# Kernel optimization log

Measured on AMD Instinct MI355X. Metric: run time of the kernel, lower is better.

Reference implementation:

```python
import jax, jax.numpy as jnp
import numpy as np

PAD_IDX = 0


def setup_inputs() -> dict:
    key = jax.random.key(0)
    ks = jax.random.split(key, 6)
    nentries, entry_size, bsize, nemb, vocab = 8000, 32, 64, 256, 50000
    keys = jax.random.randint(ks[0], (nentries,), 0, vocab)
    entries = jax.random.randint(ks[1], (nentries, entry_size), 0, vocab)
    query = jax.random.normal(ks[2], (bsize, nemb), dtype=jnp.float32)
    wordemb = jax.random.normal(ks[3], (vocab, nemb), dtype=jnp.float32)
    qproj_w = jax.random.uniform(ks[4], (nemb, nemb), jnp.float32, -0.1, 0.1)
    qproj_b = jnp.zeros((nemb,), jnp.float32)
    return dict(keys=keys, entries=entries, query=query, wordemb=wordemb,
                qproj_w=qproj_w, qproj_b=qproj_b)


def _embed(ids, wordemb):
    # F.embedding with padding_idx: gathered rows at pad_idx are zeroed
    return wordemb[ids] * (ids != PAD_IDX)[..., None].astype(wordemb.dtype)


def reference(keys, entries, query, wordemb, qproj_w, qproj_b):
    keys_e = _embed(keys, wordemb)       # (m, d)
    ents_e = _embed(entries, wordemb)    # (m, n, d)
    # --- single hop (max_hops = 1) ---
    # value_atten: query attends over the n tokens inside each entry
    vq = query @ qproj_w.T + qproj_b                       # (b, d)
    logits_v = jnp.einsum('ik,mnk->imn', vq, ents_e)       # (b, m, n)
    prob_v = jax.nn.softmax(logits_v, axis=-1)
    ents = jnp.einsum('imn,mnk->imk', prob_v, ents_e)      # (b, m, d)
    # entry_atten: query attends over entries via their keys
    logits_e = jnp.einsum('ik,jk->ij', query, keys_e)      # (b, m)
    prob_e = jax.nn.softmax(logits_e, axis=-1)
    o_k = prob_e @ keys_e                                  # (b, d)
    combined = jnp.einsum('bm,bme->be', prob_e, ents)      # (b, d)
    # return (us[-1], prob_list[-1], combined_entries)
    return o_k, logits_e, combined
```

## Files before the change

### kernel.cpp

```cpp
#include <hip/hip_runtime.h>
#include <math.h>

#define B 64
#define D 256
#define M 8000
#define N 32
#define LG_LD 8000
#define EPB 16
#define NBLK (M / EPB)
#define VOCAB 50000

typedef unsigned short u16;
typedef __bf16 bf16x8 __attribute__((ext_vector_type(8)));
typedef float fx4 __attribute__((ext_vector_type(4)));

#define STR_E  264
#define STR_P  40

static __device__ __forceinline__ u16 f2bf(float x) {
    unsigned int u = __float_as_uint(x);
    u += 0x7FFFu + ((u >> 16) & 1u);
    return (u16)(u >> 16);
}
static __device__ __forceinline__ float bf2f(u16 h) {
    return __uint_as_float(((unsigned)h) << 16);
}
static __device__ __forceinline__ uint4 pack8(float4 va, float4 vb, float msk) {
    unsigned p0 = (unsigned)f2bf(va.x * msk) | ((unsigned)f2bf(va.y * msk) << 16);
    unsigned p1 = (unsigned)f2bf(va.z * msk) | ((unsigned)f2bf(va.w * msk) << 16);
    unsigned p2 = (unsigned)f2bf(vb.x * msk) | ((unsigned)f2bf(vb.y * msk) << 16);
    unsigned p3 = (unsigned)f2bf(vb.z * msk) | ((unsigned)f2bf(vb.w * msk) << 16);
    return make_uint4(p0, p1, p2, p3);
}

__global__ __launch_bounds__(256) void k_prep_all(const int* __restrict__ keys,
                                                  const float* __restrict__ emb,
                                                  const float* __restrict__ q,
                                                  const float* __restrict__ W,
                                                  const float* __restrict__ bias,
                                                  u16* __restrict__ embb,
                                                  u16* __restrict__ qbf,
                                                  u16* __restrict__ keb,
                                                  u16* __restrict__ vqb) {
    __shared__ float qs[D];
    int t = threadIdx.x, bid = blockIdx.x;
    if (bid < 6250) {
        size_t idx = (size_t)bid * 2048 + (size_t)t * 8;
        float4 v0 = *(const float4*)(emb + idx);
        float4 v1 = *(const float4*)(emb + idx + 4);
        float msk = (idx < D) ? 0.f : 1.f;
        uint4 pk = pack8(v0, v1, msk);
        *(uint4*)(embb + idx) = pk;
    } else if (bid < 7250) {
        int c = (bid - 6250) * 256 + t;
        int j = c >> 5, sp = c & 31;
        int id = keys[j];
        const float* rp = emb + (size_t)id * D + sp * 8;
        float4 v0 = *(const float4*)rp;
        float4 v1 = *(const float4*)(rp + 4);
        float msk = (id != 0) ? 1.f : 0.f;
        uint4 pk = pack8(v0, v1, msk);
        *(uint4*)(keb + (size_t)j * D + sp * 8) = pk;
    } else if (bid < 7258) {
        size_t idx = (size_t)(bid - 7250) * 2048 + (size_t)t * 8;
        float4 v0 = *(const float4*)(q + idx);
        float4 v1 = *(const float4*)(q + idx + 4);
        uint4 pk = pack8(v0, v1, 1.f);
        *(uint4*)(qbf + idx) = pk;
    } else {
        int b = bid - 7258;
        qs[t] = q[b * D + t];
        __syncthreads();
        const float* wr = W + t * D;
        float acc = bias[t];
#pragma unroll 8
        for (int k = 0; k < D; k += 4) {
            float4 w4 = *(const float4*)(wr + k);
            acc += qs[k] * w4.x + qs[k + 1] * w4.y + qs[k + 2] * w4.z + qs[k + 3] * w4.w;
        }
        vqb[b * D + t] = f2bf(acc);
    }
}

__global__ __launch_bounds__(256, 2) void k_heavy_f(const int* __restrict__ entries,
                                                    const u16* __restrict__ embb,
                                                    const u16* __restrict__ vqb,
                                                    const u16* __restrict__ qbf,
                                                    const u16* __restrict__ keb,
                                                    float* __restrict__ lg,
                                                    u16* __restrict__ numCp,
                                                    u16* __restrict__ numKp,
                                                    float* __restrict__ mLp,
                                                    float* __restrict__ denLp) {
    __shared__ __align__(16) u16 sEu[2][N * STR_E];
    __shared__ __align__(16) u16 sETu[2][64 * 136];
    __shared__ __align__(16) u16 sPu[B * STR_P];
    __shared__ float sw[EPB][B];

    int t = threadIdx.x;
    int lane = t & 63, l = lane & 15, q = lane >> 4, w = t >> 6;
    int b0 = 16 * w;
    int sp = t & 31, n0 = t >> 5;
    int m0 = blockIdx.x * EPB;
    int bb = t & 63, y = t >> 6;

    int idc[4], idn[4];
    uint4 pfF[4];
#pragma unroll
    for (int i = 0; i < 4; ++i) idc[i] = entries[m0 * N + n0 + 8 * i];
#pragma unroll
    for (int i = 0; i < 4; ++i)
        pfF[i] = *(const uint4*)(embb + (size_t)idc[i] * D + sp * 8);

    fx4 zero4 = {0.f, 0.f, 0.f, 0.f};
    fx4 aL = zero4;
#pragma unroll
    for (int s = 0; s < 8; ++s) {
        bf16x8 a  = *(const bf16x8*)(qbf + (size_t)(b0 + l) * D + 32 * s + 8 * q);
        bf16x8 bq = *(const bf16x8*)(keb + (size_t)(m0 + l) * D + 32 * s + 8 * q);
        aL = __builtin_amdgcn_mfma_f32_16x16x32_bf16(a, bq, aL, 0, 0, 0);
    }
#pragma unroll
    for (int r = 0; r < 4; ++r)
        lg[(size_t)(b0 + 4 * q + r) * LG_LD + m0 + l] = aL[r];

#pragma unroll
    for (int r = 0; r < 4; ++r) {
        float m_ = aL[r];
        m_ = fmaxf(m_, __shfl_xor(m_, 1));
        m_ = fmaxf(m_, __shfl_xor(m_, 2));
        m_ = fmaxf(m_, __shfl_xor(m_, 4));
        m_ = fmaxf(m_, __shfl_xor(m_, 8));
        float wv = __expf(aL[r] - m_);
        sw[l][b0 + 4 * q + r] = wv;
        float d_ = wv;
        d_ += __shfl_xor(d_, 1);
        d_ += __shfl_xor(d_, 2);
        d_ += __shfl_xor(d_, 4);
        d_ += __shfl_xor(d_, 8);
        if (l == 0) {
            mLp[blockIdx.x * B + b0 + 4 * q + r] = m_;
            denLp[blockIdx.x * B + b0 + 4 * q + r] = d_;
        }
    }

    bf16x8 vqf[8];
#pragma unroll
    for (int s = 0; s < 8; ++s)
        vqf[s] = *(const bf16x8*)(vqb + (b0 + l) * D + 32 * s + 8 * q);

    fx4 acc[16];
#pragma unroll
    for (int dt = 0; dt < 16; ++dt) acc[dt] = zero4;

    {
#pragma unroll
        for (int i = 0; i < 4; ++i)
            *(uint4*)&sEu[0][(n0 + 8 * i) * STR_E + sp * 8] = pfF[i];
#pragma unroll
        for (int j = 0; j < 8; ++j) {
            unsigned a0 = (((unsigned*)&pfF[0])[j >> 1] >> ((j & 1) * 16)) & 0xFFFFu;
            unsigned a1 = (((unsigned*)&pfF[1])[j >> 1] >> ((j & 1) * 16)) & 0xFFFFu;
            unsigned a2 = (((unsigned*)&pfF[2])[j >> 1] >> ((j & 1) * 16)) & 0xFFFFu;
            unsigned a3 = (((unsigned*)&pfF[3])[j >> 1] >> ((j & 1) * 16)) & 0xFFFFu;
            uint2 pr = make_uint2(a0 | (a1 << 16), a2 | (a3 << 16));
            int off = (2 * sp + (j >> 2)) * 136 + (n0 >> 1) * 32 + (j & 3) * 8 + (n0 & 1) * 4;
            *(uint2*)&sETu[0][off] = pr;
        }
    }
#pragma unroll
    for (int i = 0; i < 4; ++i) idc[i] = entries[(m0 + 1) * N + n0 + 8 * i];
#pragma unroll
    for (int i = 0; i < 4; ++i)
        pfF[i] = *(const uint4*)(embb + (size_t)idc[i] * D + sp * 8);
#pragma unroll
    for (int i = 0; i < 4; ++i) idn[i] = entries[(m0 + 2) * N + n0 + 8 * i];

    int offL = (l >> 2) * 136 + (l & 3) * 8;

#pragma unroll 2
    for (int e = 0; e < EPB; ++e) {
        __syncthreads();
        int nxt = (e + 1) & 1;
        if (e < EPB - 1) {
#pragma unroll
            for (int i = 0; i < 4; ++i)
                *(uint4*)&sEu[nxt][(n0 + 8 * i) * STR_E + sp * 8] = pfF[i];
#pragma unroll
            for (int j = 0; j < 8; ++j) {
                unsigned a0 = (((unsigned*)&pfF[0])[j >> 1] >> ((j & 1) * 16)) & 0xFFFFu;
                unsigned a1 = (((unsigned*)&pfF[1])[j >> 1] >> ((j & 1) * 16)) & 0xFFFFu;
                unsigned a2 = (((unsigned*)&pfF[2])[j >> 1] >> ((j & 1) * 16)) & 0xFFFFu;
                unsigned a3 = (((unsigned*)&pfF[3])[j >> 1] >> ((j & 1) * 16)) & 0xFFFFu;
                uint2 pr = make_uint2(a0 | (a1 << 16), a2 | (a3 << 16));
                int off = (2 * sp + (j >> 2)) * 136 + (n0 >> 1) * 32 + (j & 3) * 8 + (n0 & 1) * 4;
                *(uint2*)&sETu[nxt][off] = pr;
            }
            if (e < EPB - 2) {
#pragma unroll
                for (int i = 0; i < 4; ++i)
                    pfF[i] = *(const uint4*)(embb + (size_t)idn[i] * D + sp * 8);
#pragma unroll
                for (int i = 0; i < 4; ++i) idc[i] = idn[i];
                if (e < EPB - 3) {
#pragma unroll
                    for (int i = 0; i < 4; ++i) idn[i] = entries[(m0 + e + 3) * N + n0 + 8 * i];
                }
            }
        }
        int cur = e & 1;
        fx4 accS[2];
        accS[0] = zero4; accS[1] = zero4;
#pragma unroll
        for (int T = 0; T < 2; ++T)
#pragma unroll
            for (int s = 0; s < 8; ++s) {
                bf16x8 ea = *(const bf16x8*)&sEu[cur][(16 * T + l) * STR_E + 32 * s + 8 * q];
                accS[T] = __builtin_amdgcn_mfma_f32_16x16x32_bf16(ea, vqf[s], accS[T], 0, 0, 0);
            }
        float swb = sw[e][b0 + l];
        float mx = -INFINITY;
#pragma unroll
        for (int T = 0; T < 2; ++T)
#pragma unroll
            for (int r = 0; r < 4; ++r) mx = fmaxf(mx, accS[T][r]);
        mx = fmaxf(mx, __shfl_xor(mx, 16));
        mx = fmaxf(mx, __shfl_xor(mx, 32));
        float pe[2][4], sum = 0.f;
#pragma unroll
        for (int T = 0; T < 2; ++T)
#pragma unroll
            for (int r = 0; r < 4; ++r) {
                pe[T][r] = __expf(accS[T][r] - mx);
                sum += pe[T][r];
            }
        sum += __shfl_xor(sum, 16);
        sum += __shfl_xor(sum, 32);
        float sc = swb / sum;
#pragma unroll
        for (int T = 0; T < 2; ++T)
#pragma unroll
            for (int r = 0; r < 4; ++r) {
                int nn = 16 * T + 4 * q + r;
                int slot = 4 * (nn & 7) + (nn >> 3);
                sPu[(b0 + l) * STR_P + slot] = f2bf(pe[T][r] * sc);
            }
        bf16x8 pa = *(const bf16x8*)&sPu[(b0 + l) * STR_P + 8 * q];
#pragma unroll
        for (int dt = 0; dt < 16; ++dt) {
            bf16x8 eb = *(const bf16x8*)&sETu[cur][offL + dt * 544 + q * 32];
            acc[dt] = __builtin_amdgcn_mfma_f32_16x16x32_bf16(pa, eb, acc[dt], 0, 0, 0);
        }
    }

    u16* ncp = numCp + (size_t)blockIdx.x * (B * D);
#pragma unroll
    for (int dt = 0; dt < 16; ++dt)
#pragma unroll
        for (int r = 0; r < 4; ++r)
            ncp[(b0 + 4 * q + r) * D + 16 * dt + l] = f2bf(acc[dt][r]);

    __syncthreads();
    {
        int rp = t >> 5;
        uint4 ka = *(const uint4*)(keb + (size_t)(m0 + rp) * D + sp * 8);
        uint4 kb = *(const uint4*)(keb + (size_t)(m0 + rp + 8) * D + sp * 8);
#pragma unroll
        for (int j = 0; j < 8; ++j) {
            unsigned a0 = (((unsigned*)&ka)[j >> 1] >> ((j & 1) * 16)) & 0xFFFFu;
            unsigned a1 = (((unsigned*)&kb)[j >> 1] >> ((j & 1) * 16)) & 0xFFFFu;
            int d = 8 * sp + j;
            int sl = 2 * rp;
            int off = (d >> 2) * 136 + (sl >> 3) * 32 + (d & 3) * 8 + (sl & 7);
            *(unsigned*)&sETu[0][off] = a0 | (a1 << 16);
        }
#pragma unroll
        for (int i = 0; i < 4; ++i) {
            int m = 4 * i + y;
            int slot = 2 * (m & 7) + (m >> 3);
            sPu[bb * STR_P + slot] = f2bf(sw[m][bb]);
        }
        *(uint2*)&sPu[bb * STR_P + 16 + 4 * y] = make_uint2(0u, 0u);
    }
    __syncthreads();
    fx4 acc2[16];
#pragma unroll
    for (int dt = 0; dt < 16; ++dt) acc2[dt] = zero4;
    {
        bf16x8 pa2 = *(const bf16x8*)&sPu[(b0 + l) * STR_P + 8 * q];
#pragma unroll
        for (int dt = 0; dt < 16; ++dt) {
            bf16x8 eb2 = *(const bf16x8*)&sETu[0][offL + dt * 544 + q * 32];
            acc2[dt] = __builtin_amdgcn_mfma_f32_16x16x32_bf16(pa2, eb2, acc2[dt], 0, 0, 0);
        }
    }
    u16* nkp = numKp + (size_t)blockIdx.x * (B * D);
#pragma unroll
    for (int dt = 0; dt < 16; ++dt)
#pragma unroll
        for (int r = 0; r < 4; ++r)
            nkp[(b0 + 4 * q + r) * D + 16 * dt + l] = f2bf(acc2[dt][r]);
}

__global__ __launch_bounds__(256) void k_comb2(const u16* __restrict__ numCp,
                                               const u16* __restrict__ numKp,
                                               const float* __restrict__ mLp,
                                               const float* __restrict__ denLp,
                                               float* __restrict__ o_k,
                                               float* __restrict__ comb) {
    __shared__ float sscale[NBLK];
    __shared__ float red[256];
    __shared__ float sro[32][33], src[32][33];
    __shared__ float srden;
    int bid = blockIdx.x;
    int b = bid >> 3, d0 = (bid & 7) * 32;
    int t = threadIdx.x;
    float mx = -INFINITY;
    for (int blk = t; blk < NBLK; blk += 256) mx = fmaxf(mx, mLp[blk * B + b]);
    red[t] = mx;
    __syncthreads();
    for (int s = 128; s > 0; s >>= 1) {
        if (t < s) red[t] = fmaxf(red[t], red[t + s]);
        __syncthreads();
    }
    float Mg = red[0];
    __syncthreads();
    float ds = 0.f;
    for (int blk = t; blk < NBLK; blk += 256) {
        float sc = __expf(mLp[blk * B + b] - Mg);
        sscale[blk] = sc;
        ds += sc * denLp[blk * B + b];
    }
    red[t] = ds;
    __syncthreads();
    for (int s = 128; s > 0; s >>= 1) {
        if (t < s) red[t] += red[t + s];
        __syncthreads();
    }
    if (t == 0) srden = 1.f / red[0];
    __syncthreads();
    int v = t & 7, s = t >> 3;
    float ao[4] = {0.f, 0.f, 0.f, 0.f}, ac[4] = {0.f, 0.f, 0.f, 0.f};
    for (int blk = s; blk < NBLK; blk += 32) {
        float sc = sscale[blk];
        size_t i = (size_t)blk * (B * D) + (size_t)b * D + d0 + v * 4;
        uint2 kk = *(const uint2*)(numKp + i);
        uint2 cc = *(const uint2*)(numCp + i);
        ao[0] += sc * bf2f((u16)(kk.x & 0xFFFFu));
        ao[1] += sc * bf2f((u16)(kk.x >> 16));
        ao[2] += sc * bf2f((u16)(kk.y & 0xFFFFu));
        ao[3] += sc * bf2f((u16)(kk.y >> 16));
        ac[0] += sc * bf2f((u16)(cc.x & 0xFFFFu));
        ac[1] += sc * bf2f((u16)(cc.x >> 16));
        ac[2] += sc * bf2f((u16)(cc.y & 0xFFFFu));
        ac[3] += sc * bf2f((u16)(cc.y >> 16));
    }
#pragma unroll
    for (int k = 0; k < 4; ++k) {
        sro[s][v * 4 + k] = ao[k];
        src[s][v * 4 + k] = ac[k];
    }
    __syncthreads();
    if (t < 32) {
        float so = 0.f, sc2 = 0.f;
#pragma unroll
        for (int k2 = 0; k2 < 32; ++k2) { so += sro[k2][t]; sc2 += src[k2][t]; }
        float rd = srden;
        o_k[b * D + d0 + t] = so * rd;
        comb[b * D + d0 + t] = sc2 * rd;
    }
}


extern "C" void kernel_launch(void* const* d_in, const int* in_sizes, int n_in,
                              void* d_out, int out_size, void* d_ws, size_t ws_size,
                              hipStream_t stream) {
    const int*   keys    = (const int*)d_in[0];
    const int*   entries = (const int*)d_in[1];
    const float* query   = (const float*)d_in[2];
    const float* wordemb = (const float*)d_in[3];
    const float* qproj_w = (const float*)d_in[4];
    const float* qproj_b = (const float*)d_in[5];

    float* out  = (float*)d_out;
    float* o_k  = out;
    float* lg   = out + B * D;
    float* comb = out + B * D + B * M;

    char* wsb = (char*)d_ws;
    u16*   embb  = (u16*)wsb;
    u16*   keb   = (u16*)(wsb + 25600000);
    u16*   qbf   = (u16*)(wsb + 29696000);
    u16*   vqb   = (u16*)(wsb + 29728768);
    u16*   numCp = (u16*)(wsb + 29761536);
    u16*   numKp = (u16*)(wsb + 46145536);
    float* mLp   = (float*)(wsb + 62529536);
    float* denLp = (float*)(wsb + 62657536);

    k_prep_all<<<7322, 256, 0, stream>>>(keys, wordemb, query, qproj_w, qproj_b,
                                         embb, qbf, keb, vqb);
    k_heavy_f<<<NBLK, 256, 0, stream>>>(entries, embb, vqb, qbf, keb, lg,
                                        numCp, numKp, mLp, denLp);
    k_comb2<<<512, 256, 0, stream>>>(numCp, numKp, mLp, denLp, o_k, comb);
}
```

Before: 171.8 us.

## Single-buffer LDS in heavy kernel, halve entries per block, raise occupancy

The heavy kernel drops double-buffered LDS for single buffers with two barriers per entry, and stores entry weights as bf16 to cut shared memory so four blocks can fit per CU. When the workspace is large enough it launches 1000 blocks of 8 entries instead of 500 blocks of 16, using a templated combine kernel over more partials. The prep kernel zero-pads extra keb rows so the 16-row key MFMA tile stays in bounds. The trade-off is lost LDS overlap of staging with compute, and more partial-sum traffic in the combine step.

```diff
diff --git a/kernel.cpp b/kernel.cpp
--- a/kernel.cpp
+++ b/kernel.cpp
@@ -6,8 +6,6 @@
 #define M 8000
 #define N 32
 #define LG_LD 8000
-#define EPB 16
-#define NBLK (M / EPB)
 #define VOCAB 50000
 
 typedef unsigned short u16;
@@ -32,6 +30,12 @@
     unsigned p3 = (unsigned)f2bf(vb.z * msk) | ((unsigned)f2bf(vb.w * msk) << 16);
     return make_uint4(p0, p1, p2, p3);
 }
+
+#define BARRIER_LGKM() do {                                   \
+    asm volatile("s_waitcnt lgkmcnt(0)" ::: "memory");        \
+    __builtin_amdgcn_s_barrier();                             \
+    asm volatile("" ::: "memory");                            \
+} while (0)
 
 __global__ __launch_bounds__(256) void k_prep_all(const int* __restrict__ keys,
                                                   const float* __restrict__ emb,
@@ -67,7 +71,7 @@
         float4 v1 = *(const float4*)(q + idx + 4);
         uint4 pk = pack8(v0, v1, 1.f);
         *(uint4*)(qbf + idx) = pk;
-    } else {
+    } else if (bid < 7322) {
         int b = bid - 7258;
         qs[t] = q[b * D + t];
         __syncthreads();
@@ -79,10 +83,14 @@
             acc += qs[k] * w4.x + qs[k + 1] * w4.y + qs[k + 2] * w4.z + qs[k + 3] * w4.w;
         }
         vqb[b * D + t] = f2bf(acc);
-    }
-}
-
-__global__ __launch_bounds__(256, 2) void k_heavy_f(const int* __restrict__ entries,
+    } else {
+        int idx = (bid - 7322) * 256 + t;
+        *(uint4*)(keb + (size_t)8000 * D + (size_t)idx * 8) = make_uint4(0u, 0u, 0u, 0u);
+    }
+}
+
+template <int EPB_>
+__global__ __launch_bounds__(256, 4) void k_heavy_s(const int* __restrict__ entries,
                                                     const u16* __restrict__ embb,
                                                     const u16* __restrict__ vqb,
                                                     const u16* __restrict__ qbf,
@@ -92,25 +100,25 @@
                                                     u16* __restrict__ numKp,
                                                     float* __restrict__ mLp,
                                                     float* __restrict__ denLp) {
-    __shared__ __align__(16) u16 sEu[2][N * STR_E];
-    __shared__ __align__(16) u16 sETu[2][64 * 136];
+    __shared__ __align__(16) u16 sEu[N * STR_E];
+    __shared__ __align__(16) u16 sETu[64 * 136];
     __shared__ __align__(16) u16 sPu[B * STR_P];
-    __shared__ float sw[EPB][B];
+    __shared__ u16 sw16[EPB_][B];
 
     int t = threadIdx.x;
     int lane = t & 63, l = lane & 15, q = lane >> 4, w = t >> 6;
     int b0 = 16 * w;
     int sp = t & 31, n0 = t >> 5;
-    int m0 = blockIdx.x * EPB;
+    int m0 = blockIdx.x * EPB_;
     int bb = t & 63, y = t >> 6;
 
-    int idc[4], idn[4];
+    int idn[4];
     uint4 pfF[4];
 #pragma unroll
-    for (int i = 0; i < 4; ++i) idc[i] = entries[m0 * N + n0 + 8 * i];
+    for (int i = 0; i < 4; ++i) idn[i] = entries[m0 * N + n0 + 8 * i];
 #pragma unroll
     for (int i = 0; i < 4; ++i)
-        pfF[i] = *(const uint4*)(embb + (size_t)idc[i] * D + sp * 8);
+        pfF[i] = *(const uint4*)(embb + (size_t)idn[i] * D + sp * 8);
 
     fx4 zero4 = {0.f, 0.f, 0.f, 0.f};
     fx4 aL = zero4;
@@ -120,20 +128,23 @@
         bf16x8 bq = *(const bf16x8*)(keb + (size_t)(m0 + l) * D + 32 * s + 8 * q);
         aL = __builtin_amdgcn_mfma_f32_16x16x32_bf16(a, bq, aL, 0, 0, 0);
     }
-#pragma unroll
-    for (int r = 0; r < 4; ++r)
-        lg[(size_t)(b0 + 4 * q + r) * LG_LD + m0 + l] = aL[r];
+    if (l < EPB_) {
+#pragma unroll
+        for (int r = 0; r < 4; ++r)
+            lg[(size_t)(b0 + 4 * q + r) * LG_LD + m0 + l] = aL[r];
+    }
 
 #pragma unroll
     for (int r = 0; r < 4; ++r) {
-        float m_ = aL[r];
+        float v = (l < EPB_) ? aL[r] : -INFINITY;
+        float m_ = v;
         m_ = fmaxf(m_, __shfl_xor(m_, 1));
         m_ = fmaxf(m_, __shfl_xor(m_, 2));
         m_ = fmaxf(m_, __shfl_xor(m_, 4));
         m_ = fmaxf(m_, __shfl_xor(m_, 8));
         float wv = __expf(aL[r] - m_);
-        sw[l][b0 + 4 * q + r] = wv;
-        float d_ = wv;
+        if (l < EPB_) sw16[l][b0 + 4 * q + r] = f2bf(wv);
+        float d_ = (l < EPB_) ? wv : 0.f;
         d_ += __shfl_xor(d_, 1);
         d_ += __shfl_xor(d_, 2);
         d_ += __shfl_xor(d_, 4);
@@ -156,7 +167,7 @@
     {
 #pragma unroll
         for (int i = 0; i < 4; ++i)
-            *(uint4*)&sEu[0][(n0 + 8 * i) * STR_E + sp * 8] = pfF[i];
+            *(uint4*)&sEu[(n0 + 8 * i) * STR_E + sp * 8] = pfF[i];
 #pragma unroll
         for (int j = 0; j < 8; ++j) {
             unsigned a0 = (((unsigned*)&pfF[0])[j >> 1] >> ((j & 1) * 16)) & 0xFFFFu;
@@ -165,27 +176,69 @@
             unsigned a3 = (((unsigned*)&pfF[3])[j >> 1] >> ((j & 1) * 16)) & 0xFFFFu;
             uint2 pr = make_uint2(a0 | (a1 << 16), a2 | (a3 << 16));
             int off = (2 * sp + (j >> 2)) * 136 + (n0 >> 1) * 32 + (j & 3) * 8 + (n0 & 1) * 4;
-            *(uint2*)&sETu[0][off] = pr;
-        }
-    }
-#pragma unroll
-    for (int i = 0; i < 4; ++i) idc[i] = entries[(m0 + 1) * N + n0 + 8 * i];
+            *(uint2*)&sETu[off] = pr;
+        }
+    }
+#pragma unroll
+    for (int i = 0; i < 4; ++i) idn[i] = entries[(m0 + 1) * N + n0 + 8 * i];
 #pragma unroll
     for (int i = 0; i < 4; ++i)
-        pfF[i] = *(const uint4*)(embb + (size_t)idc[i] * D + sp * 8);
+        pfF[i] = *(const uint4*)(embb + (size_t)idn[i] * D + sp * 8);
 #pragma unroll
     for (int i = 0; i < 4; ++i) idn[i] = entries[(m0 + 2) * N + n0 + 8 * i];
 
     int offL = (l >> 2) * 136 + (l & 3) * 8;
 
 #pragma unroll 2
-    for (int e = 0; e < EPB; ++e) {
-        __syncthreads();
-        int nxt = (e + 1) & 1;
-        if (e < EPB - 1) {
+    for (int e = 0; e < EPB_; ++e) {
+        BARRIER_LGKM();
+        fx4 accS[2];
+        accS[0] = zero4; accS[1] = zero4;
+#pragma unroll
+        for (int T = 0; T < 2; ++T)
+#pragma unroll
+            for (int s = 0; s < 8; ++s) {
+                bf16x8 ea = *(const bf16x8*)&sEu[(16 * T + l) * STR_E + 32 * s + 8 * q];
+                accS[T] = __builtin_amdgcn_mfma_f32_16x16x32_bf16(ea, vqf[s], accS[T], 0, 0, 0);
+            }
+        float swb = bf2f(sw16[e][b0 + l]);
+        float mx = -INFINITY;
+#pragma unroll
+        for (int T = 0; T < 2; ++T)
+#pragma unroll
+            for (int r = 0; r < 4; ++r) mx = fmaxf(mx, accS[T][r]);
+        mx = fmaxf(mx, __shfl_xor(mx, 16));
+        mx = fmaxf(mx, __shfl_xor(mx, 32));
+        float pe[2][4], sum = 0.f;
+#pragma unroll
+        for (int T = 0; T < 2; ++T)
+#pragma unroll
+            for (int r = 0; r < 4; ++r) {
+                pe[T][r] = __expf(accS[T][r] - mx);
+                sum += pe[T][r];
+            }
+        sum += __shfl_xor(sum, 16);
+        sum += __shfl_xor(sum, 32);
+        float sc = swb / sum;
+#pragma unroll
+        for (int T = 0; T < 2; ++T)
+#pragma unroll
+            for (int r = 0; r < 4; ++r) {
+                int nn = 16 * T + 4 * q + r;
+                int slot = 4 * (nn & 7) + (nn >> 3);
+                sPu[(b0 + l) * STR_P + slot] = f2bf(pe[T][r] * sc);
+            }
+        bf16x8 pa = *(const bf16x8*)&sPu[(b0 + l) * STR_P + 8 * q];
+#pragma unroll
+        for (int dt = 0; dt < 16; ++dt) {
+            bf16x8 eb = *(const bf16x8*)&sETu[offL + dt * 544 + q * 32];
+            acc[dt] = __builtin_amdgcn_mfma_f32_16x16x32_bf16(pa, eb, acc[dt], 0, 0, 0);
+        }
+        BARRIER_LGKM();
+        if (e < EPB_ - 1) {
 #pragma unroll
             for (int i = 0; i < 4; ++i)
-                *(uint4*)&sEu[nxt][(n0 + 8 * i) * STR_E + sp * 8] = pfF[i];
+                *(uint4*)&sEu[(n0 + 8 * i) * STR_E + sp * 8] = pfF[i];
 #pragma unroll
             for (int j = 0; j < 8; ++j) {
                 unsigned a0 = (((unsigned*)&pfF[0])[j >> 1] >> ((j & 1) * 16)) & 0xFFFFu;
@@ -194,63 +247,18 @@
                 unsigned a3 = (((unsigned*)&pfF[3])[j >> 1] >> ((j & 1) * 16)) & 0xFFFFu;
                 uint2 pr = make_uint2(a0 | (a1 << 16), a2 | (a3 << 16));
                 int off = (2 * sp + (j >> 2)) * 136 + (n0 >> 1) * 32 + (j & 3) * 8 + (n0 & 1) * 4;
-                *(uint2*)&sETu[nxt][off] = pr;
+                *(uint2*)&sETu[off] = pr;
             }
-            if (e < EPB - 2) {
+            if (e < EPB_ - 2) {
 #pragma unroll
                 for (int i = 0; i < 4; ++i)
                     pfF[i] = *(const uint4*)(embb + (size_t)idn[i] * D + sp * 8);
-#pragma unroll
-                for (int i = 0; i < 4; ++i) idc[i] = idn[i];
-                if (e < EPB - 3) {
+                if (e < EPB_ - 3) {
 #pragma unroll
                     for (int i = 0; i < 4; ++i) idn[i] = entries[(m0 + e + 3) * N + n0 + 8 * i];
                 }
             }
         }
-        int cur = e & 1;
-        fx4 accS[2];
-        accS[0] = zero4; accS[1] = zero4;
-#pragma unroll
-        for (int T = 0; T < 2; ++T)
-#pragma unroll
-            for (int s = 0; s < 8; ++s) {
-                bf16x8 ea = *(const bf16x8*)&sEu[cur][(16 * T + l) * STR_E + 32 * s + 8 * q];
-                accS[T] = __builtin_amdgcn_mfma_f32_16x16x32_bf16(ea, vqf[s], accS[T], 0, 0, 0);
-            }
-        float swb = sw[e][b0 + l];
-        float mx = -INFINITY;
-#pragma unroll
-        for (int T = 0; T < 2; ++T)
-#pragma unroll
-            for (int r = 0; r < 4; ++r) mx = fmaxf(mx, accS[T][r]);
-        mx = fmaxf(mx, __shfl_xor(mx, 16));
-        mx = fmaxf(mx, __shfl_xor(mx, 32));
-        float pe[2][4], sum = 0.f;
-#pragma unroll
-        for (int T = 0; T < 2; ++T)
-#pragma unroll
-            for (int r = 0; r < 4; ++r) {
-                pe[T][r] = __expf(accS[T][r] - mx);
-                sum += pe[T][r];
-            }
-        sum += __shfl_xor(sum, 16);
-        sum += __shfl_xor(sum, 32);
-        float sc = swb / sum;
-#pragma unroll
-        for (int T = 0; T < 2; ++T)
-#pragma unroll
-            for (int r = 0; r < 4; ++r) {
-                int nn = 16 * T + 4 * q + r;
-                int slot = 4 * (nn & 7) + (nn >> 3);
-                sPu[(b0 + l) * STR_P + slot] = f2bf(pe[T][r] * sc);
-            }
-        bf16x8 pa = *(const bf16x8*)&sPu[(b0 + l) * STR_P + 8 * q];
-#pragma unroll
-        for (int dt = 0; dt < 16; ++dt) {
-            bf16x8 eb = *(const bf16x8*)&sETu[cur][offL + dt * 544 + q * 32];
-            acc[dt] = __builtin_amdgcn_mfma_f32_16x16x32_bf16(pa, eb, acc[dt], 0, 0, 0);
-        }
     }
 
     u16* ncp = numCp + (size_t)blockIdx.x * (B * D);
@@ -260,8 +268,8 @@
         for (int r = 0; r < 4; ++r)
             ncp[(b0 + 4 * q + r) * D + 16 * dt + l] = f2bf(acc[dt][r]);
 
-    __syncthreads();
-    {
+    BARRIER_LGKM();
+    if constexpr (EPB_ == 16) {
         int rp = t >> 5;
         uint4 ka = *(const uint4*)(keb + (size_t)(m0 + rp) * D + sp * 8);
         uint4 kb = *(const uint4*)(keb + (size_t)(m0 + rp + 8) * D + sp * 8);
@@ -272,17 +280,34 @@
             int d = 8 * sp + j;
             int sl = 2 * rp;
             int off = (d >> 2) * 136 + (sl >> 3) * 32 + (d & 3) * 8 + (sl & 7);
-            *(unsigned*)&sETu[0][off] = a0 | (a1 << 16);
+            *(unsigned*)&sETu[off] = a0 | (a1 << 16);
         }
 #pragma unroll
         for (int i = 0; i < 4; ++i) {
             int m = 4 * i + y;
             int slot = 2 * (m & 7) + (m >> 3);
-            sPu[bb * STR_P + slot] = f2bf(sw[m][bb]);
+            sPu[bb * STR_P + slot] = sw16[m][bb];
         }
         *(uint2*)&sPu[bb * STR_P + 16 + 4 * y] = make_uint2(0u, 0u);
-    }
-    __syncthreads();
+    } else {
+        int rp = t >> 5;
+        uint4 ka = *(const uint4*)(keb + (size_t)(m0 + rp) * D + sp * 8);
+#pragma unroll
+        for (int j = 0; j < 8; ++j) {
+            unsigned a0 = (((unsigned*)&ka)[j >> 1] >> ((j & 1) * 16)) & 0xFFFFu;
+            int d = 8 * sp + j;
+            int sl = 2 * rp;
+            int off = (d >> 2) * 136 + (sl >> 3) * 32 + (d & 3) * 8 + (sl & 7);
+            *(unsigned*)&sETu[off] = a0;
+        }
+#pragma unroll
+        for (int j = 0; j < 4; ++j) {
+            unsigned val = 0u;
+            if (y < 2) val = (unsigned)sw16[4 * y + j][bb];
+            *(unsigned*)&sPu[bb * STR_P + 8 * y + 2 * j] = val;
+        }
+    }
+    BARRIER_LGKM();
     fx4 acc2[16];
 #pragma unroll
     for (int dt = 0; dt < 16; ++dt) acc2[dt] = zero4;
@@ -290,7 +315,7 @@
         bf16x8 pa2 = *(const bf16x8*)&sPu[(b0 + l) * STR_P + 8 * q];
 #pragma unroll
         for (int dt = 0; dt < 16; ++dt) {
-            bf16x8 eb2 = *(const bf16x8*)&sETu[0][offL + dt * 544 + q * 32];
+            bf16x8 eb2 = *(const bf16x8*)&sETu[offL + dt * 544 + q * 32];
             acc2[dt] = __builtin_amdgcn_mfma_f32_16x16x32_bf16(pa2, eb2, acc2[dt], 0, 0, 0);
         }
     }
@@ -302,13 +327,14 @@
             nkp[(b0 + 4 * q + r) * D + 16 * dt + l] = f2bf(acc2[dt][r]);
 }
 
-__global__ __launch_bounds__(256) void k_comb2(const u16* __restrict__ numCp,
-                                               const u16* __restrict__ numKp,
-                                               const float* __restrict__ mLp,
-                                               const float* __restrict__ denLp,
-                                               float* __restrict__ o_k,
-                                               float* __restrict__ comb) {
-    __shared__ float sscale[NBLK];
+template <int NBLK_>
+__global__ __launch_bounds__(256) void k_comb2t(const u16* __restrict__ numCp,
+                                                const u16* __restrict__ numKp,
+                                                const float* __restrict__ mLp,
+                                                const float* __restrict__ denLp,
+                                                float* __restrict__ o_k,
+                                                float* __restrict__ comb) {
+    __shared__ float sscale[NBLK_];
     __shared__ float red[256];
     __shared__ float sro[32][33], src[32][33];
     __shared__ float srden;
@@ -316,7 +342,7 @@
     int b = bid >> 3, d0 = (bid & 7) * 32;
     int t = threadIdx.x;
     float mx = -INFINITY;
-    for (int blk = t; blk < NBLK; blk += 256) mx = fmaxf(mx, mLp[blk * B + b]);
+    for (int blk = t; blk < NBLK_; blk += 256) mx = fmaxf(mx, mLp[blk * B + b]);
     red[t] = mx;
     __syncthreads();
     for (int s = 128; s > 0; s >>= 1) {
@@ -326,7 +352,7 @@
     float Mg = red[0];
     __syncthreads();
     float ds = 0.f;
-    for (int blk = t; blk < NBLK; blk += 256) {
+    for (int blk = t; blk < NBLK_; blk += 256) {
         float sc = __expf(mLp[blk * B + b] - Mg);
         sscale[blk] = sc;
         ds += sc * denLp[blk * B + b];
@@ -341,7 +367,7 @@
     __syncthreads();
     int v = t & 7, s = t >> 3;
     float ao[4] = {0.f, 0.f, 0.f, 0.f}, ac[4] = {0.f, 0.f, 0.f, 0.f};
-    for (int blk = s; blk < NBLK; blk += 32) {
+    for (int blk = s; blk < NBLK_; blk += 32) {
         float sc = sscale[blk];
         size_t i = (size_t)blk * (B * D) + (size_t)b * D + d0 + v * 4;
         uint2 kk = *(const uint2*)(numKp + i);
@@ -388,18 +414,35 @@
     float* comb = out + B * D + B * M;
 
     char* wsb = (char*)d_ws;
-    u16*   embb  = (u16*)wsb;
-    u16*   keb   = (u16*)(wsb + 25600000);
-    u16*   qbf   = (u16*)(wsb + 29696000);
-    u16*   vqb   = (u16*)(wsb + 29728768);
-    u16*   numCp = (u16*)(wsb + 29761536);
-    u16*   numKp = (u16*)(wsb + 46145536);
-    float* mLp   = (float*)(wsb + 62529536);
-    float* denLp = (float*)(wsb + 62657536);
-
-    k_prep_all<<<7322, 256, 0, stream>>>(keys, wordemb, query, qproj_w, qproj_b,
+    u16* embb = (u16*)wsb;
+    u16* keb  = (u16*)(wsb + 25600000);
+    u16* qbf  = (u16*)(wsb + 29704192);
+    u16* vqb  = (u16*)(wsb + 29736960);
+    char* dyn = wsb + 29769728;
+
+    const size_t szC8 = (size_t)1000 * B * D * 2;
+    const size_t szS8 = (size_t)1000 * B * 4;
+    const size_t need8 = 29769728 + 2 * szC8 + 2 * szS8;
+
+    k_prep_all<<<7324, 256, 0, stream>>>(keys, wordemb, query, qproj_w, qproj_b,
                                          embb, qbf, keb, vqb);
-    k_heavy_f<<<NBLK, 256, 0, stream>>>(entries, embb, vqb, qbf, keb, lg,
-                                        numCp, numKp, mLp, denLp);
-    k_comb2<<<512, 256, 0, stream>>>(numCp, numKp, mLp, denLp, o_k, comb);
-}
+    if (ws_size >= need8) {
+        u16*   numCp = (u16*)dyn;
+        u16*   numKp = (u16*)(dyn + szC8);
+        float* mLp   = (float*)(dyn + 2 * szC8);
+        float* denLp = (float*)(dyn + 2 * szC8 + szS8);
+        k_heavy_s<8><<<1000, 256, 0, stream>>>(entries, embb, vqb, qbf, keb, lg,
+                                               numCp, numKp, mLp, denLp);
+        k_comb2t<1000><<<512, 256, 0, stream>>>(numCp, numKp, mLp, denLp, o_k, comb);
+    } else {
+        const size_t szC = (size_t)500 * B * D * 2;
+        const size_t szS = (size_t)500 * B * 4;
+        u16*   numCp = (u16*)dyn;
+        u16*   numKp = (u16*)(dyn + szC);
+        float* mLp   = (float*)(dyn + 2 * szC);
+        float* denLp = (float*)(dyn + 2 * szC + szS);
+        k_heavy_s<16><<<500, 256, 0, stream>>>(entries, embb, vqb, qbf, keb, lg,
+                                               numCp, numKp, mLp, denLp);
+        k_comb2t<500><<<512, 256, 0, stream>>>(numCp, numKp, mLp, denLp, o_k, comb);
+    }
+}
```

Result: slower. 261.0 us (+51.9%).

## Retile PV MFMA so each wave covers all batch rows for a quarter of D

Applied to the files above, without the earlier changes.

The second MFMA stage (probabilities times entry embeddings) now has each wave compute all 64 batch rows for its own 64-column slice of D, instead of 16 batch rows across all of D. Each B-operand fragment loaded from LDS is reused across four MFMAs, cutting LDS reads of the transposed entry tile. The transposed-tile layout is swizzled to match. Because waves now read probability rows written by other waves, an explicit lgkmcnt wait plus barrier is added each iteration, which adds synchronisation cost.

```diff
diff --git a/kernel.cpp b/kernel.cpp
--- a/kernel.cpp
+++ b/kernel.cpp
@@ -32,6 +32,12 @@
     unsigned p3 = (unsigned)f2bf(vb.z * msk) | ((unsigned)f2bf(vb.w * msk) << 16);
     return make_uint4(p0, p1, p2, p3);
 }
+
+#define BARRIER_LGKM() do {                                   \
+    asm volatile("s_waitcnt lgkmcnt(0)" ::: "memory");        \
+    __builtin_amdgcn_s_barrier();                             \
+    asm volatile("" ::: "memory");                            \
+} while (0)
 
 __global__ __launch_bounds__(256) void k_prep_all(const int* __restrict__ keys,
                                                   const float* __restrict__ emb,
@@ -164,7 +170,7 @@
             unsigned a2 = (((unsigned*)&pfF[2])[j >> 1] >> ((j & 1) * 16)) & 0xFFFFu;
             unsigned a3 = (((unsigned*)&pfF[3])[j >> 1] >> ((j & 1) * 16)) & 0xFFFFu;
             uint2 pr = make_uint2(a0 | (a1 << 16), a2 | (a3 << 16));
-            int off = (2 * sp + (j >> 2)) * 136 + (n0 >> 1) * 32 + (j & 3) * 8 + (n0 & 1) * 4;
+            int off = (2 * sp + (j >> 2)) * 136 + (j & 3) * 32 + (n0 >> 1) * 8 + (n0 & 1) * 4;
             *(uint2*)&sETu[0][off] = pr;
         }
     }
@@ -176,7 +182,7 @@
 #pragma unroll
     for (int i = 0; i < 4; ++i) idn[i] = entries[(m0 + 2) * N + n0 + 8 * i];
 
-    int offL = (l >> 2) * 136 + (l & 3) * 8;
+    int offL2 = (l >> 2) * 136 + (l & 3) * 32;
 
 #pragma unroll 2
     for (int e = 0; e < EPB; ++e) {
@@ -193,7 +199,7 @@
                 unsigned a2 = (((unsigned*)&pfF[2])[j >> 1] >> ((j & 1) * 16)) & 0xFFFFu;
                 unsigned a3 = (((unsigned*)&pfF[3])[j >> 1] >> ((j & 1) * 16)) & 0xFFFFu;
                 uint2 pr = make_uint2(a0 | (a1 << 16), a2 | (a3 << 16));
-                int off = (2 * sp + (j >> 2)) * 136 + (n0 >> 1) * 32 + (j & 3) * 8 + (n0 & 1) * 4;
+                int off = (2 * sp + (j >> 2)) * 136 + (j & 3) * 32 + (n0 >> 1) * 8 + (n0 & 1) * 4;
                 *(uint2*)&sETu[nxt][off] = pr;
             }
             if (e < EPB - 2) {
@@ -245,20 +251,32 @@
                 int slot = 4 * (nn & 7) + (nn >> 3);
                 sPu[(b0 + l) * STR_P + slot] = f2bf(pe[T][r] * sc);
             }
-        bf16x8 pa = *(const bf16x8*)&sPu[(b0 + l) * STR_P + 8 * q];
-#pragma unroll
-        for (int dt = 0; dt < 16; ++dt) {
-            bf16x8 eb = *(const bf16x8*)&sETu[cur][offL + dt * 544 + q * 32];
-            acc[dt] = __builtin_amdgcn_mfma_f32_16x16x32_bf16(pa, eb, acc[dt], 0, 0, 0);
+        BARRIER_LGKM();
+        {
+            bf16x8 paA[4];
+#pragma unroll
+            for (int bg = 0; bg < 4; ++bg)
+                paA[bg] = *(const bf16x8*)&sPu[(16 * bg + l) * STR_P + 8 * q];
+#pragma unroll
+            for (int dtl = 0; dtl < 4; ++dtl) {
+                bf16x8 eb = *(const bf16x8*)&sETu[cur][offL2 + (4 * w + dtl) * 544 + q * 8];
+#pragma unroll
+                for (int bg = 0; bg < 4; ++bg)
+                    acc[4 * bg + dtl] = __builtin_amdgcn_mfma_f32_16x16x32_bf16(
+                        paA[bg], eb, acc[4 * bg + dtl], 0, 0, 0);
+            }
         }
     }
 
     u16* ncp = numCp + (size_t)blockIdx.x * (B * D);
 #pragma unroll
-    for (int dt = 0; dt < 16; ++dt)
-#pragma unroll
-        for (int r = 0; r < 4; ++r)
-            ncp[(b0 + 4 * q + r) * D + 16 * dt + l] = f2bf(acc[dt][r]);
+    for (int bg = 0; bg < 4; ++bg)
+#pragma unroll
+        for (int dtl = 0; dtl < 4; ++dtl)
+#pragma unroll
+            for (int r = 0; r < 4; ++r)
+                ncp[(16 * bg + 4 * q + r) * D + 16 * (4 * w + dtl) + l] =
+                    f2bf(acc[4 * bg + dtl][r]);
 
     __syncthreads();
     {
@@ -271,7 +289,7 @@
             unsigned a1 = (((unsigned*)&kb)[j >> 1] >> ((j & 1) * 16)) & 0xFFFFu;
             int d = 8 * sp + j;
             int sl = 2 * rp;
-            int off = (d >> 2) * 136 + (sl >> 3) * 32 + (d & 3) * 8 + (sl & 7);
+            int off = (d >> 2) * 136 + (d & 3) * 32 + (sl >> 3) * 8 + (sl & 7);
             *(unsigned*)&sETu[0][off] = a0 | (a1 << 16);
         }
 #pragma unroll
@@ -287,19 +305,28 @@
 #pragma unroll
     for (int dt = 0; dt < 16; ++dt) acc2[dt] = zero4;
     {
-        bf16x8 pa2 = *(const bf16x8*)&sPu[(b0 + l) * STR_P + 8 * q];
-#pragma unroll
-        for (int dt = 0; dt < 16; ++dt) {
-            bf16x8 eb2 = *(const bf16x8*)&sETu[0][offL + dt * 544 + q * 32];
-            acc2[dt] = __builtin_amdgcn_mfma_f32_16x16x32_bf16(pa2, eb2, acc2[dt], 0, 0, 0);
+        bf16x8 pa2A[4];
+#pragma unroll
+        for (int bg = 0; bg < 4; ++bg)
+            pa2A[bg] = *(const bf16x8*)&sPu[(16 * bg + l) * STR_P + 8 * q];
+#pragma unroll
+        for (int dtl = 0; dtl < 4; ++dtl) {
+            bf16x8 eb2 = *(const bf16x8*)&sETu[0][offL2 + (4 * w + dtl) * 544 + q * 8];
+#pragma unroll
+            for (int bg = 0; bg < 4; ++bg)
+                acc2[4 * bg + dtl] = __builtin_amdgcn_mfma_f32_16x16x32_bf16(
+                    pa2A[bg], eb2, acc2[4 * bg + dtl], 0, 0, 0);
         }
     }
     u16* nkp = numKp + (size_t)blockIdx.x * (B * D);
 #pragma unroll
-    for (int dt = 0; dt < 16; ++dt)
-#pragma unroll
-        for (int r = 0; r < 4; ++r)
-            nkp[(b0 + 4 * q + r) * D + 16 * dt + l] = f2bf(acc2[dt][r]);
+    for (int bg = 0; bg < 4; ++bg)
+#pragma unroll
+        for (int dtl = 0; dtl < 4; ++dtl)
+#pragma unroll
+            for (int r = 0; r < 4; ++r)
+                nkp[(16 * bg + 4 * q + r) * D + 16 * (4 * w + dtl) + l] =
+                    f2bf(acc2[4 * bg + dtl][r]);
 }
 
 __global__ __launch_bounds__(256) void k_comb2(const u16* __restrict__ numCp,
```

Result: faster. 168.2 us (-2.1%).
